# Performance work log

Hardware: AMD Instinct MI355X
Metric: run time of the kernel (lower is better)

The kernel has to match this reference:

```python
import jax, jax.numpy as jnp
import numpy as np

TOP_K = 2
EPS = 1e-6

def setup_inputs() -> dict:
    B, S, H, G, E, M = 2, 2048, 1024, 256, 8, 2048
    key = jax.random.key(0)
    ks = jax.random.split(key, 16)
    s_h = 1.0 / np.sqrt(H)
    s_g = 1.0 / np.sqrt(G)
    s_m = 1.0 / np.sqrt(M)
    return {
        "x": jax.random.normal(ks[0], (B, S, H), jnp.float32),
        "genre_embed": jax.random.normal(ks[1], (B, 1, G), jnp.float32),
        "rms_w": jnp.ones((H,), jnp.float32),
        "wg_W": jax.random.normal(ks[2], (H, E), jnp.float32) * s_h,
        "wg_b": jnp.zeros((E,), jnp.float32),
        "gg_W": jax.random.normal(ks[3], (G, E), jnp.float32) * s_g,
        "gg_b": jnp.zeros((E,), jnp.float32),
        "W1": jax.random.normal(ks[4], (E, H, M), jnp.float32) * s_h,
        "b1": jnp.zeros((E, M), jnp.float32),
        "W2": jax.random.normal(ks[5], (E, M, M), jnp.float32) * s_m,
        "b2": jnp.zeros((E, M), jnp.float32),
        "W3": jax.random.normal(ks[6], (E, M, H), jnp.float32) * s_m,
        "b3": jnp.zeros((E, H), jnp.float32),
    }


def reference(x, genre_embed, rms_w, wg_W, wg_b, gg_W, gg_b, W1, b1, W2, b2, W3, b3):
    E = W1.shape[0]
    # RMSNorm
    var = jnp.mean(x * x, axis=-1, keepdims=True)
    xn = rms_w * (x * jax.lax.rsqrt(var + EPS))
    # gating: word gate [B,S,E] + genre gate [B,1,E] (broadcast over seq)
    gate = (xn @ wg_W + wg_b) + (genre_embed @ gg_W + gg_b)
    gate_w = jax.nn.softmax(gate, axis=-1)
    topk_w, topk_i = jax.lax.top_k(gate_w, TOP_K)  # [B,S,K]
    # combine weights per expert: sum_k topk_w * onehot(topk_i)
    cw = jnp.sum(jax.nn.one_hot(topk_i, E, dtype=x.dtype) * topk_w[..., None], axis=-2)  # [B,S,E]
    # dense all-expert MLP (equivalent math to masked dispatch/combine)
    h1 = jax.nn.relu(jnp.einsum('bsh,ehm->bsem', x, W1) + b1)
    h2 = jax.nn.relu(jnp.einsum('bsem,emn->bsen', h1, W2) + b2)
    out_e = jnp.einsum('bsen,enh->bseh', h2, W3) + b3
    return jnp.einsum('bseh,bse->bsh', out_e, cw)
```

## Files before the change

kernel.cpp:

```cpp
#include <hip/hip_runtime.h>
#include <hip/hip_bf16.h>

#define T_TOK 4096
#define N_PAIR 8192
#define H_DIM 1024
#define M_DIM 2048
#define E_NUM 8

#define T_W1 4096
#define T_W2 8192
#define T_W3 4096
#define T_ROUT 1024

using bf16x8 = __attribute__((ext_vector_type(8))) short;
using f32x4  = __attribute__((ext_vector_type(4))) float;

__device__ __forceinline__ unsigned short f2bf(float f) {
    unsigned int u = __builtin_bit_cast(unsigned int, f);
    u += 0x7fffu + ((u >> 16) & 1u);
    return (unsigned short)(u >> 16);
}
__device__ __forceinline__ float bf2f(unsigned short u) {
    return __builtin_bit_cast(float, (unsigned int)u << 16);
}

__device__ __forceinline__ void async16(const unsigned short* g, unsigned short* l) {
    __builtin_amdgcn_global_load_lds(
        (const __attribute__((address_space(1))) void*)g,
        (__attribute__((address_space(3))) void*)l, 16, 0, 0);
}

__global__ void k_prep(const float* __restrict__ W1, const float* __restrict__ W2,
                       const float* __restrict__ W3,
                       unsigned short* __restrict__ W1t, unsigned short* __restrict__ W2t,
                       unsigned short* __restrict__ W3t,
                       const float* __restrict__ x, const float* __restrict__ rms_w,
                       const float* __restrict__ wg_W, const float* __restrict__ genre,
                       const float* __restrict__ gg_W, const float* __restrict__ gg_b,
                       const float* __restrict__ wg_b,
                       int* __restrict__ tok_e, float* __restrict__ tok_w)
{
    __shared__ float ld[32][132];
    int bid = blockIdx.x;

    if (bid < T_W1 + T_W2 + T_W3) {
        const float* W; unsigned short* Wt; int tile, kshift, ntshift, N, K;
        if (bid < T_W1)              { W = W1; Wt = W1t; tile = bid;                 K = H_DIM; N = M_DIM; kshift = 10; ntshift = 4; }
        else if (bid < T_W1 + T_W2)  { W = W2; Wt = W2t; tile = bid - T_W1;          K = M_DIM; N = M_DIM; kshift = 11; ntshift = 4; }
        else                         { W = W3; Wt = W3t; tile = bid - T_W1 - T_W2;   K = M_DIM; N = H_DIM; kshift = 11; ntshift = 3; }
        int r0 = (tile >> ntshift) * 32;
        int n0 = (tile & ((1 << ntshift) - 1)) * 128;
        int t = threadIdx.x;
        {
            int rr = t >> 3, c0 = t & 7;
            const float4* src = (const float4*)(W + (size_t)(r0 + rr) * N + n0);
#pragma unroll
            for (int cc = 0; cc < 4; cc++) {
                float4 v = src[c0 + cc * 8];
                float* d = &ld[rr][(c0 + cc * 8) * 4];
                d[0] = v.x; d[1] = v.y; d[2] = v.z; d[3] = v.w;
            }
        }
        __syncthreads();
        {
            int n = t >> 1, half = t & 1;
            int kb = half * 16;
            bf16x8 o0, o1;
#pragma unroll
            for (int q = 0; q < 8; q++) o0[q] = (short)f2bf(ld[kb + q][n]);
#pragma unroll
            for (int q = 0; q < 8; q++) o1[q] = (short)f2bf(ld[kb + 8 + q][n]);
            int rg = r0 + kb;
            int e = rg >> kshift;
            int k = rg & (K - 1);
            unsigned short* dst = Wt + ((size_t)e * N + (n0 + n)) * K + k;
            *(bf16x8*)dst = o0;
            *(bf16x8*)(dst + 8) = o1;
        }
        return;
    }

    int wave = threadIdx.x >> 6, lane = threadIdx.x & 63;
    int tok = (bid - (T_W1 + T_W2 + T_W3)) * 4 + wave;
    int b = tok >> 11;
    const float* xr = x + (size_t)tok * H_DIM;
    float xv[16];
    float ss = 0.f;
#pragma unroll
    for (int j = 0; j < 16; j++) { xv[j] = xr[lane + 64 * j]; ss += xv[j] * xv[j]; }
#pragma unroll
    for (int off = 32; off > 0; off >>= 1) ss += __shfl_xor(ss, off);
    float rstd = rsqrtf(ss * (1.f / 1024.f) + 1e-6f);
    float g[8] = {0.f, 0.f, 0.f, 0.f, 0.f, 0.f, 0.f, 0.f};
#pragma unroll
    for (int gi0 = 0; gi0 < 4; gi0++) {
        int gi = lane + gi0 * 64;
        float gf = genre[b * 256 + gi];
        const float4* w4 = (const float4*)(gg_W + gi * 8);
        float4 wa = w4[0], wb = w4[1];
        g[0] += gf * wa.x; g[1] += gf * wa.y; g[2] += gf * wa.z; g[3] += gf * wa.w;
        g[4] += gf * wb.x; g[5] += gf * wb.y; g[6] += gf * wb.z; g[7] += gf * wb.w;
    }
#pragma unroll
    for (int j = 0; j < 16; j++) {
        int h = lane + 64 * j;
        float xn = xv[j] * rstd * rms_w[h];
        const float4* w4 = (const float4*)(wg_W + h * 8);
        float4 wa = w4[0], wb = w4[1];
        g[0] += xn * wa.x; g[1] += xn * wa.y; g[2] += xn * wa.z; g[3] += xn * wa.w;
        g[4] += xn * wb.x; g[5] += xn * wb.y; g[6] += xn * wb.z; g[7] += xn * wb.w;
    }
#pragma unroll
    for (int e = 0; e < 8; e++) {
#pragma unroll
        for (int off = 32; off > 0; off >>= 1) g[e] += __shfl_xor(g[e], off);
    }
    if (lane == 0) {
#pragma unroll
        for (int e = 0; e < 8; e++) g[e] += wg_b[e] + gg_b[e];
        float m = g[0];
        for (int e = 1; e < 8; e++) m = fmaxf(m, g[e]);
        float p[8], psum = 0.f;
        for (int e = 0; e < 8; e++) { p[e] = expf(g[e] - m); psum += p[e]; }
        int i0 = 0;
        for (int e = 1; e < 8; e++) if (p[e] > p[i0]) i0 = e;
        int i1 = (i0 == 0) ? 1 : 0;
        for (int e = 0; e < 8; e++) if (e != i0 && p[e] > p[i1]) i1 = e;
        float inv = 1.f / psum;
        tok_e[tok * 2] = i0;         tok_e[tok * 2 + 1] = i1;
        tok_w[tok * 2] = p[i0] * inv; tok_w[tok * 2 + 1] = p[i1] * inv;
    }
}

__global__ void k_scan(const int* __restrict__ tok_e, int* __restrict__ meta)
{
    __shared__ int cnt[8];
    int t = threadIdx.x;
    if (t < 8) cnt[t] = 0;
    __syncthreads();
    for (int p = t; p < N_PAIR; p += 256) atomicAdd(&cnt[tok_e[p]], 1);
    __syncthreads();
    if (t == 0) {
        int acc = 0;
        for (int e = 0; e < 8; e++) {
            meta[e] = cnt[e]; meta[8 + e] = acc; meta[16 + e] = acc; acc += cnt[e];
        }
    }
}

__global__ void k_gather(const float* __restrict__ x, const int* __restrict__ tok_e,
                         int* __restrict__ meta, int* __restrict__ pair_pos,
                         unsigned short* __restrict__ x_g)
{
    int wave = threadIdx.x >> 6, lane = threadIdx.x & 63;
    int p = blockIdx.x * 4 + wave;
    int t = p >> 1;
    int e = tok_e[p];
    int pos;
    if (lane == 0) {
        pos = atomicAdd(&meta[16 + e], 1);
        pair_pos[p] = pos;
    }
    pos = __shfl(pos, 0);
    const float4* src = (const float4*)(x + (size_t)t * H_DIM);
    ushort4* dst = (ushort4*)(x_g + (size_t)pos * H_DIM);
#pragma unroll
    for (int j = 0; j < 4; j++) {
        float4 v = src[lane + 64 * j];
        ushort4 o;
        o.x = f2bf(v.x); o.y = f2bf(v.y); o.z = f2bf(v.z); o.w = f2bf(v.w);
        dst[lane + 64 * j] = o;
    }
}

template<bool RELU>
__global__ void k_gemm(const unsigned short* __restrict__ A,
                       const unsigned short* __restrict__ Wt,
                       const float* __restrict__ bias,
                       unsigned short* __restrict__ C,
                       const int* __restrict__ meta,
                       int K, int N)
{
    int e = blockIdx.z;
    int cnt = meta[e];
    int by = blockIdx.y;
    if (by * 128 >= cnt) return;
    int base = meta[8 + e];
    int bx = blockIdx.x;

    __shared__ __align__(16) unsigned short As[128 * 64];
    __shared__ __align__(16) unsigned short Bs[128 * 64];

    int tid = threadIdx.x;
    int wave = tid >> 6, lane = tid & 63;
    int lrow8 = lane >> 3;
    int lslot = lane & 7;
    int chunk_g = (lslot ^ lrow8) * 8;

    const unsigned short* Bw = Wt + (size_t)e * N * K + (size_t)(bx * 128) * K;
    const unsigned short* gA[4]; const unsigned short* gB[4];
    unsigned short* lA[4]; unsigned short* lB[4];
#pragma unroll
    for (int c = 0; c < 4; c++) {
        int rloc = wave * 32 + c * 8 + lrow8;
        int ra = base + by * 128 + rloc;
        ra = min(ra, N_PAIR - 1);
        gA[c] = A + (size_t)ra * K + chunk_g;
        gB[c] = Bw + (size_t)rloc * K + chunk_g;
        lA[c] = &As[(wave * 32 + c * 8) * 64];
        lB[c] = &Bs[(wave * 32 + c * 8) * 64];
    }

    int wr = (wave >> 1) * 64, wc = (wave & 1) * 64;
    int lm = lane & 15, lq = lane >> 4;

    int aoff[4][2], boff[4][2];
#pragma unroll
    for (int i = 0; i < 4; i++)
#pragma unroll
        for (int h = 0; h < 2; h++) {
            int R = wr + i * 16 + lm;
            aoff[i][h] = R * 64 + (((h * 4 + lq) ^ (R & 7)) * 8);
            int Nn = wc + i * 16 + lm;
            boff[i][h] = Nn * 64 + (((h * 4 + lq) ^ (Nn & 7)) * 8);
        }

    f32x4 acc[4][4] = {};

    for (int kt = 0; kt < K; kt += 64) {
#pragma unroll
        for (int c = 0; c < 4; c++) { async16(gA[c] + kt, lA[c]); async16(gB[c] + kt, lB[c]); }
        __syncthreads();
#pragma unroll
        for (int h = 0; h < 2; h++) {
            bf16x8 af[4], bfr[4];
#pragma unroll
            for (int i = 0; i < 4; i++) af[i] = *(const bf16x8*)&As[aoff[i][h]];
#pragma unroll
            for (int j = 0; j < 4; j++) bfr[j] = *(const bf16x8*)&Bs[boff[j][h]];
#pragma unroll
            for (int i = 0; i < 4; i++)
#pragma unroll
                for (int j = 0; j < 4; j++)
                    acc[i][j] = __builtin_amdgcn_mfma_f32_16x16x32_bf16(af[i], bfr[j], acc[i][j], 0, 0, 0);
        }
        __syncthreads();
    }

#pragma unroll
    for (int j = 0; j < 4; j++) {
        int n = bx * 128 + wc + j * 16 + lm;
        float bv = bias[(size_t)e * N + n];
#pragma unroll
        for (int i = 0; i < 4; i++) {
#pragma unroll
            for (int r = 0; r < 4; r++) {
                int grow = by * 128 + wr + i * 16 + lq * 4 + r;
                if (grow < cnt) {
                    float v = acc[i][j][r] + bv;
                    if (RELU) v = fmaxf(v, 0.f);
                    C[(size_t)(base + grow) * N + n] = f2bf(v);
                }
            }
        }
    }
}

__global__ void k_combine(const unsigned short* __restrict__ o3,
                          const int* __restrict__ pair_pos,
                          const float* __restrict__ tok_w, float* __restrict__ out)
{
    int t = blockIdx.x;
    int c = threadIdx.x;
    int p0 = pair_pos[t * 2], p1 = pair_pos[t * 2 + 1];
    float w0 = tok_w[t * 2], w1 = tok_w[t * 2 + 1];
    ushort4 a = ((const ushort4*)(o3 + (size_t)p0 * H_DIM))[c];
    ushort4 bq = ((const ushort4*)(o3 + (size_t)p1 * H_DIM))[c];
    float4 o;
    o.x = w0 * bf2f(a.x) + w1 * bf2f(bq.x);
    o.y = w0 * bf2f(a.y) + w1 * bf2f(bq.y);
    o.z = w0 * bf2f(a.z) + w1 * bf2f(bq.z);
    o.w = w0 * bf2f(a.w) + w1 * bf2f(bq.w);
    ((float4*)(out + (size_t)t * H_DIM))[c] = o;
}

extern "C" void kernel_launch(void* const* d_in, const int* in_sizes, int n_in,
                              void* d_out, int out_size, void* d_ws, size_t ws_size,
                              hipStream_t stream) {
    const float* x      = (const float*)d_in[0];
    const float* genre  = (const float*)d_in[1];
    const float* rms_w  = (const float*)d_in[2];
    const float* wg_W   = (const float*)d_in[3];
    const float* wg_b   = (const float*)d_in[4];
    const float* gg_W   = (const float*)d_in[5];
    const float* gg_b   = (const float*)d_in[6];
    const float* W1     = (const float*)d_in[7];
    const float* b1     = (const float*)d_in[8];
    const float* W2     = (const float*)d_in[9];
    const float* b2     = (const float*)d_in[10];
    const float* W3     = (const float*)d_in[11];
    const float* b3     = (const float*)d_in[12];
    float* out = (float*)d_out;

    char* p = (char*)d_ws;
    auto alloc = [&](size_t bytes) { char* r = p; p += (bytes + 255) & ~(size_t)255; return r; };
    unsigned short* W1t = (unsigned short*)alloc((size_t)E_NUM * H_DIM * M_DIM * 2);
    unsigned short* W2t = (unsigned short*)alloc((size_t)E_NUM * M_DIM * M_DIM * 2);
    unsigned short* W3t = (unsigned short*)alloc((size_t)E_NUM * M_DIM * H_DIM * 2);
    unsigned short* x_g = (unsigned short*)alloc((size_t)N_PAIR * H_DIM * 2);
    unsigned short* h1  = (unsigned short*)alloc((size_t)N_PAIR * M_DIM * 2);
    unsigned short* h2  = (unsigned short*)alloc((size_t)N_PAIR * M_DIM * 2);
    unsigned short* o3  = (unsigned short*)alloc((size_t)N_PAIR * H_DIM * 2);
    int*   meta         = (int*)alloc(24 * 4);
    int*   tok_e        = (int*)alloc((size_t)N_PAIR * 4);
    float* tok_w        = (float*)alloc((size_t)N_PAIR * 4);
    int*   pair_pos     = (int*)alloc((size_t)N_PAIR * 4);

    dim3 blk(256);

    k_prep<<<T_W1 + T_W2 + T_W3 + T_ROUT, blk, 0, stream>>>(
        W1, W2, W3, W1t, W2t, W3t, x, rms_w, wg_W, genre, gg_W, gg_b, wg_b,
        tok_e, tok_w);
    k_scan<<<1, blk, 0, stream>>>(tok_e, meta);
    k_gather<<<N_PAIR / 4, blk, 0, stream>>>(x, tok_e, meta, pair_pos, x_g);

    k_gemm<true ><<<dim3(M_DIM / 128, 32, E_NUM), blk, 0, stream>>>(
        x_g, W1t, b1, h1, meta, H_DIM, M_DIM);
    k_gemm<true ><<<dim3(M_DIM / 128, 32, E_NUM), blk, 0, stream>>>(
        h1, W2t, b2, h2, meta, M_DIM, M_DIM);
    k_gemm<false><<<dim3(H_DIM / 128, 32, E_NUM), blk, 0, stream>>>(
        h2, W3t, b3, o3, meta, M_DIM, H_DIM);

    k_combine<<<T_TOK, blk, 0, stream>>>(o3, pair_pos, tok_w, out);

    (void)in_sizes; (void)n_in; (void)ws_size;
}
```

Measured before the change: 699.4 us.

## Overlap W2/W3 conversion with first expert GEMM and gather rows via permutation

The W2/W3 fp32-to-bf16 transposes move out of the prep kernel into a combined kernel that interleaves them with the first expert GEMM blocks, so that weight conversion overlaps MFMA work. The separate gather kernel is removed. Prep now writes one bf16 copy of x per token, the scan builds a token permutation, and the first GEMM loads A rows indirectly through that permutation. Transpose tiles change from 32x128 to 64x64. This drops one launch and the duplicated x_g write, but makes the first GEMM's A loads irregular and ties its schedule to the transpose blocks sharing the grid.

```diff
diff --git a/kernel.cpp b/kernel.cpp
--- a/kernel.cpp
+++ b/kernel.cpp
@@ -30,64 +30,68 @@
         (__attribute__((address_space(3))) void*)l, 16, 0, 0);
 }
 
-__global__ void k_prep(const float* __restrict__ W1, const float* __restrict__ W2,
-                       const float* __restrict__ W3,
-                       unsigned short* __restrict__ W1t, unsigned short* __restrict__ W2t,
-                       unsigned short* __restrict__ W3t,
+__device__ __forceinline__ void transpose_tile(const float* __restrict__ W,
+                                               unsigned short* __restrict__ Wt,
+                                               int tile, int K, int N,
+                                               int kshift, int ntshift, char* smemraw)
+{
+    float (*ld)[68] = (float (*)[68])smemraw;
+    int r0 = (tile >> ntshift) * 64;
+    int n0 = (tile & ((1 << ntshift) - 1)) * 64;
+    int t = threadIdx.x;
+    {
+        int row = t >> 2, c0 = t & 3;
+        const float4* src = (const float4*)(W + (size_t)(r0 + row) * N + n0);
+#pragma unroll
+        for (int c = 0; c < 4; c++) {
+            float4 v = src[c0 + 4 * c];
+            float* d = &ld[row][(c0 + 4 * c) * 4];
+            d[0] = v.x; d[1] = v.y; d[2] = v.z; d[3] = v.w;
+        }
+    }
+    __syncthreads();
+    {
+        int n = t >> 2, k0 = (t & 3) * 16;
+        bf16x8 o0, o1;
+#pragma unroll
+        for (int q = 0; q < 8; q++) o0[q] = (short)f2bf(ld[k0 + q][n]);
+#pragma unroll
+        for (int q = 0; q < 8; q++) o1[q] = (short)f2bf(ld[k0 + 8 + q][n]);
+        int e = r0 >> kshift;
+        int k = (r0 & (K - 1)) + k0;
+        unsigned short* dst = Wt + ((size_t)e * N + (n0 + n)) * K + k;
+        *(bf16x8*)dst = o0;
+        *(bf16x8*)(dst + 8) = o1;
+    }
+}
+
+__global__ void k_prep(const float* __restrict__ W1, unsigned short* __restrict__ W1t,
                        const float* __restrict__ x, const float* __restrict__ rms_w,
                        const float* __restrict__ wg_W, const float* __restrict__ genre,
                        const float* __restrict__ gg_W, const float* __restrict__ gg_b,
                        const float* __restrict__ wg_b,
-                       int* __restrict__ tok_e, float* __restrict__ tok_w)
-{
-    __shared__ float ld[32][132];
+                       int* __restrict__ tok_e, float* __restrict__ tok_w,
+                       unsigned short* __restrict__ xb)
+{
+    __shared__ __align__(16) char smem[17408];
     int bid = blockIdx.x;
 
-    if (bid < T_W1 + T_W2 + T_W3) {
-        const float* W; unsigned short* Wt; int tile, kshift, ntshift, N, K;
-        if (bid < T_W1)              { W = W1; Wt = W1t; tile = bid;                 K = H_DIM; N = M_DIM; kshift = 10; ntshift = 4; }
-        else if (bid < T_W1 + T_W2)  { W = W2; Wt = W2t; tile = bid - T_W1;          K = M_DIM; N = M_DIM; kshift = 11; ntshift = 4; }
-        else                         { W = W3; Wt = W3t; tile = bid - T_W1 - T_W2;   K = M_DIM; N = H_DIM; kshift = 11; ntshift = 3; }
-        int r0 = (tile >> ntshift) * 32;
-        int n0 = (tile & ((1 << ntshift) - 1)) * 128;
-        int t = threadIdx.x;
-        {
-            int rr = t >> 3, c0 = t & 7;
-            const float4* src = (const float4*)(W + (size_t)(r0 + rr) * N + n0);
-#pragma unroll
-            for (int cc = 0; cc < 4; cc++) {
-                float4 v = src[c0 + cc * 8];
-                float* d = &ld[rr][(c0 + cc * 8) * 4];
-                d[0] = v.x; d[1] = v.y; d[2] = v.z; d[3] = v.w;
-            }
-        }
-        __syncthreads();
-        {
-            int n = t >> 1, half = t & 1;
-            int kb = half * 16;
-            bf16x8 o0, o1;
-#pragma unroll
-            for (int q = 0; q < 8; q++) o0[q] = (short)f2bf(ld[kb + q][n]);
-#pragma unroll
-            for (int q = 0; q < 8; q++) o1[q] = (short)f2bf(ld[kb + 8 + q][n]);
-            int rg = r0 + kb;
-            int e = rg >> kshift;
-            int k = rg & (K - 1);
-            unsigned short* dst = Wt + ((size_t)e * N + (n0 + n)) * K + k;
-            *(bf16x8*)dst = o0;
-            *(bf16x8*)(dst + 8) = o1;
-        }
+    if (bid < T_W1) {
+        transpose_tile(W1, W1t, bid, H_DIM, M_DIM, 10, 5, smem);
         return;
     }
 
     int wave = threadIdx.x >> 6, lane = threadIdx.x & 63;
-    int tok = (bid - (T_W1 + T_W2 + T_W3)) * 4 + wave;
+    int tok = (bid - T_W1) * 4 + wave;
     int b = tok >> 11;
     const float* xr = x + (size_t)tok * H_DIM;
+    unsigned short* xs = (unsigned short*)smem;
     float xv[16];
     float ss = 0.f;
 #pragma unroll
     for (int j = 0; j < 16; j++) { xv[j] = xr[lane + 64 * j]; ss += xv[j] * xv[j]; }
+#pragma unroll
+    for (int j = 0; j < 16; j++) xs[wave * 1024 + lane + 64 * j] = f2bf(xv[j]);
 #pragma unroll
     for (int off = 32; off > 0; off >>= 1) ss += __shfl_xor(ss, off);
     float rstd = rsqrtf(ss * (1.f / 1024.f) + 1e-6f);
@@ -114,6 +118,14 @@
     for (int e = 0; e < 8; e++) {
 #pragma unroll
         for (int off = 32; off > 0; off >>= 1) g[e] += __shfl_xor(g[e], off);
+    }
+    __syncthreads();
+    {
+        unsigned short* dst = xb + (size_t)tok * H_DIM;
+        bf16x8 a0 = *(bf16x8*)&xs[wave * 1024 + lane * 16];
+        bf16x8 a1 = *(bf16x8*)&xs[wave * 1024 + lane * 16 + 8];
+        *(bf16x8*)(dst + lane * 16) = a0;
+        *(bf16x8*)(dst + lane * 16 + 8) = a1;
     }
     if (lane == 0) {
 #pragma unroll
@@ -132,9 +144,10 @@
     }
 }
 
-__global__ void k_scan(const int* __restrict__ tok_e, int* __restrict__ meta)
-{
-    __shared__ int cnt[8];
+__global__ void k_scan(const int* __restrict__ tok_e, int* __restrict__ meta,
+                       int* __restrict__ perm, int* __restrict__ pair_pos)
+{
+    __shared__ int cnt[8], fill[8];
     int t = threadIdx.x;
     if (t < 8) cnt[t] = 0;
     __syncthreads();
@@ -143,33 +156,113 @@
     if (t == 0) {
         int acc = 0;
         for (int e = 0; e < 8; e++) {
-            meta[e] = cnt[e]; meta[8 + e] = acc; meta[16 + e] = acc; acc += cnt[e];
-        }
-    }
-}
-
-__global__ void k_gather(const float* __restrict__ x, const int* __restrict__ tok_e,
-                         int* __restrict__ meta, int* __restrict__ pair_pos,
-                         unsigned short* __restrict__ x_g)
-{
-    int wave = threadIdx.x >> 6, lane = threadIdx.x & 63;
-    int p = blockIdx.x * 4 + wave;
-    int t = p >> 1;
-    int e = tok_e[p];
-    int pos;
-    if (lane == 0) {
-        pos = atomicAdd(&meta[16 + e], 1);
+            meta[e] = cnt[e]; meta[8 + e] = acc; fill[e] = acc; acc += cnt[e];
+        }
+    }
+    __syncthreads();
+    for (int p = t; p < N_PAIR; p += 256) {
+        int e = tok_e[p];
+        int pos = atomicAdd(&fill[e], 1);
+        perm[pos] = p >> 1;
         pair_pos[p] = pos;
     }
-    pos = __shfl(pos, 0);
-    const float4* src = (const float4*)(x + (size_t)t * H_DIM);
-    ushort4* dst = (ushort4*)(x_g + (size_t)pos * H_DIM);
+}
+
+__global__ void k_mlp1(const float* __restrict__ W2, const float* __restrict__ W3,
+                       unsigned short* __restrict__ W2t, unsigned short* __restrict__ W3t,
+                       const unsigned short* __restrict__ xb,
+                       const unsigned short* __restrict__ W1t,
+                       const float* __restrict__ b1, unsigned short* __restrict__ h1,
+                       const int* __restrict__ meta, const int* __restrict__ perm)
+{
+    __shared__ __align__(16) char smem[32768];
+    int id = blockIdx.x;
+    int sel = id & 3;
+    if (sel != 3) {
+        int t_idx = (id >> 2) * 3 + sel;
+        if (t_idx < T_W2) transpose_tile(W2, W2t, t_idx, M_DIM, M_DIM, 11, 5, smem);
+        else              transpose_tile(W3, W3t, t_idx - T_W2, M_DIM, H_DIM, 11, 4, smem);
+        return;
+    }
+    int g = id >> 2;
+    int bx = g & 15, by = (g >> 4) & 31, e = g >> 9;
+    int cnt = meta[e];
+    if (by * 128 >= cnt) return;
+    int base = meta[8 + e];
+    const int K = H_DIM, N = M_DIM;
+
+    unsigned short* As = (unsigned short*)smem;
+    unsigned short* Bs = (unsigned short*)(smem + 16384);
+
+    int tid = threadIdx.x;
+    int wave = tid >> 6, lane = tid & 63;
+    int lrow8 = lane >> 3;
+    int lslot = lane & 7;
+    int chunk_g = (lslot ^ lrow8) * 8;
+
+    const unsigned short* Bw = W1t + (size_t)e * N * K + (size_t)(bx * 128) * K;
+    const unsigned short* gA[4]; const unsigned short* gB[4];
+    unsigned short* lA[4]; unsigned short* lB[4];
+#pragma unroll
+    for (int c = 0; c < 4; c++) {
+        int rloc = wave * 32 + c * 8 + lrow8;
+        int grow = by * 128 + rloc;
+        int tok = (grow < cnt) ? perm[base + grow] : 0;
+        gA[c] = xb + (size_t)tok * K + chunk_g;
+        gB[c] = Bw + (size_t)rloc * K + chunk_g;
+        lA[c] = &As[(wave * 32 + c * 8) * 64];
+        lB[c] = &Bs[(wave * 32 + c * 8) * 64];
+    }
+
+    int wr = (wave >> 1) * 64, wc = (wave & 1) * 64;
+    int lm = lane & 15, lq = lane >> 4;
+    int aoff[4][2], boff[4][2];
+#pragma unroll
+    for (int i = 0; i < 4; i++)
+#pragma unroll
+        for (int h = 0; h < 2; h++) {
+            int R = wr + i * 16 + lm;
+            aoff[i][h] = R * 64 + (((h * 4 + lq) ^ (R & 7)) * 8);
+            int Nn = wc + i * 16 + lm;
+            boff[i][h] = Nn * 64 + (((h * 4 + lq) ^ (Nn & 7)) * 8);
+        }
+
+    f32x4 acc[4][4] = {};
+    for (int kt = 0; kt < K; kt += 64) {
+#pragma unroll
+        for (int c = 0; c < 4; c++) { async16(gA[c] + kt, lA[c]); async16(gB[c] + kt, lB[c]); }
+        __syncthreads();
+#pragma unroll
+        for (int h = 0; h < 2; h++) {
+            bf16x8 af[4], bfr[4];
+#pragma unroll
+            for (int i = 0; i < 4; i++) af[i] = *(const bf16x8*)&As[aoff[i][h]];
+#pragma unroll
+            for (int j = 0; j < 4; j++) bfr[j] = *(const bf16x8*)&Bs[boff[j][h]];
+#pragma unroll
+            for (int i = 0; i < 4; i++)
+#pragma unroll
+                for (int j = 0; j < 4; j++)
+                    acc[i][j] = __builtin_amdgcn_mfma_f32_16x16x32_bf16(af[i], bfr[j], acc[i][j], 0, 0, 0);
+        }
+        __syncthreads();
+    }
+
 #pragma unroll
     for (int j = 0; j < 4; j++) {
-        float4 v = src[lane + 64 * j];
-        ushort4 o;
-        o.x = f2bf(v.x); o.y = f2bf(v.y); o.z = f2bf(v.z); o.w = f2bf(v.w);
-        dst[lane + 64 * j] = o;
+        int n = bx * 128 + wc + j * 16 + lm;
+        float bv = b1[(size_t)e * N + n];
+#pragma unroll
+        for (int i = 0; i < 4; i++) {
+#pragma unroll
+            for (int r = 0; r < 4; r++) {
+                int grow = by * 128 + wr + i * 16 + lq * 4 + r;
+                if (grow < cnt) {
+                    float v = fmaxf(acc[i][j][r] + bv, 0.f);
+                    h1[(size_t)(base + grow) * N + n] = f2bf(v);
+                }
+            }
+        }
     }
 }
 
@@ -213,7 +306,6 @@
 
     int wr = (wave >> 1) * 64, wc = (wave & 1) * 64;
     int lm = lane & 15, lq = lane >> 4;
-
     int aoff[4][2], boff[4][2];
 #pragma unroll
     for (int i = 0; i < 4; i++)
@@ -226,7 +318,6 @@
         }
 
     f32x4 acc[4][4] = {};
-
     for (int kt = 0; kt < K; kt += 64) {
 #pragma unroll
         for (int c = 0; c < 4; c++) { async16(gA[c] + kt, lA[c]); async16(gB[c] + kt, lB[c]); }
@@ -307,30 +398,26 @@
     unsigned short* W1t = (unsigned short*)alloc((size_t)E_NUM * H_DIM * M_DIM * 2);
     unsigned short* W2t = (unsigned short*)alloc((size_t)E_NUM * M_DIM * M_DIM * 2);
     unsigned short* W3t = (unsigned short*)alloc((size_t)E_NUM * M_DIM * H_DIM * 2);
-    unsigned short* x_g = (unsigned short*)alloc((size_t)N_PAIR * H_DIM * 2);
+    unsigned short* xb  = (unsigned short*)alloc((size_t)T_TOK * H_DIM * 2);
     unsigned short* h1  = (unsigned short*)alloc((size_t)N_PAIR * M_DIM * 2);
     unsigned short* h2  = (unsigned short*)alloc((size_t)N_PAIR * M_DIM * 2);
     unsigned short* o3  = (unsigned short*)alloc((size_t)N_PAIR * H_DIM * 2);
-    int*   meta         = (int*)alloc(24 * 4);
+    int*   meta         = (int*)alloc(16 * 4);
     int*   tok_e        = (int*)alloc((size_t)N_PAIR * 4);
     float* tok_w        = (float*)alloc((size_t)N_PAIR * 4);
+    int*   perm         = (int*)alloc((size_t)N_PAIR * 4);
     int*   pair_pos     = (int*)alloc((size_t)N_PAIR * 4);
 
     dim3 blk(256);
 
-    k_prep<<<T_W1 + T_W2 + T_W3 + T_ROUT, blk, 0, stream>>>(
-        W1, W2, W3, W1t, W2t, W3t, x, rms_w, wg_W, genre, gg_W, gg_b, wg_b,
-        tok_e, tok_w);
-    k_scan<<<1, blk, 0, stream>>>(tok_e, meta);
-    k_gather<<<N_PAIR / 4, blk, 0, stream>>>(x, tok_e, meta, pair_pos, x_g);
-
-    k_gemm<true ><<<dim3(M_DIM / 128, 32, E_NUM), blk, 0, stream>>>(
-        x_g, W1t, b1, h1, meta, H_DIM, M_DIM);
+    k_prep<<<T_W1 + T_ROUT, blk, 0, stream>>>(
+        W1, W1t, x, rms_w, wg_W, genre, gg_W, gg_b, wg_b, tok_e, tok_w, xb);
+    k_scan<<<1, blk, 0, stream>>>(tok_e, meta, perm, pair_pos);
+    k_mlp1<<<16384, blk, 0, stream>>>(W2, W3, W2t, W3t, xb, W1t, b1, h1, meta, perm);
     k_gemm<true ><<<dim3(M_DIM / 128, 32, E_NUM), blk, 0, stream>>>(
         h1, W2t, b2, h2, meta, M_DIM, M_DIM);
     k_gemm<false><<<dim3(H_DIM / 128, 32, E_NUM), blk, 0, stream>>>(
         h2, W3t, b3, o3, meta, M_DIM, H_DIM);
-
     k_combine<<<T_TOK, blk, 0, stream>>>(o3, pair_pos, tok_w, out);
 
     (void)in_sizes; (void)n_in; (void)ws_size;
```

Result: slower. 758.9 us (+8.5%).
